# Kernel tuning notes

Hardware: AMD Instinct MI355X
Metric: run time of the kernel (lower is better)

## Reference

```python
import jax, jax.numpy as jnp
import numpy as np

N_NODES = 20000
N_EDGES = 160000
EPS = 1e-5
LEAKY_SLOPE = 0.01


def gcn_conv(x, src, dst, W, b, num_nodes):
    """PyG GCNConv: self-loops + symmetric normalization. out = D^-1/2 A_hat D^-1/2 (x W) + b."""
    h = x @ W  # [N, out]
    loop = jnp.arange(num_nodes, dtype=src.dtype)
    s = jnp.concatenate([src, loop])
    d = jnp.concatenate([dst, loop])
    deg = jax.ops.segment_sum(jnp.ones_like(d, dtype=h.dtype), d, num_segments=num_nodes)
    dinv = jnp.where(deg > 0, jax.lax.rsqrt(jnp.maximum(deg, 1.0)) * jnp.where(deg > 0, 1.0, 0.0), 0.0)
    norm = dinv[s] * dinv[d]  # [E+N]
    msgs = h[s] * norm[:, None]  # gather + scale (memory-bound)
    out = jax.ops.segment_sum(msgs, d, num_segments=num_nodes)
    return out + b


def setup_inputs() -> dict:
    key = jax.random.key(0)
    ks = jax.random.split(key, 8)
    x = jax.random.normal(ks[0], (N_NODES, 1), dtype=jnp.float32)
    edge_index = jax.random.randint(ks[1], (2, N_EDGES), 0, N_NODES, dtype=jnp.int32)
    s = 0.02
    W1 = jax.random.normal(ks[2], (1, 2048), dtype=jnp.float32) * s
    b1 = jnp.zeros((2048,), jnp.float32)
    W2 = jax.random.normal(ks[3], (2048, 1024), dtype=jnp.float32) * s
    b2 = jnp.zeros((1024,), jnp.float32)
    gamma = jnp.ones((1024,), jnp.float32)
    beta = jnp.zeros((1024,), jnp.float32)
    running_mean = jnp.zeros((1024,), jnp.float32)
    running_var = jnp.ones((1024,), jnp.float32)
    lW1 = jax.random.normal(ks[4], (1024, 256), dtype=jnp.float32) * s
    lb1 = jnp.zeros((256,), jnp.float32)
    lW2 = jax.random.normal(ks[5], (256, 124), dtype=jnp.float32) * s
    lb2 = jnp.zeros((124,), jnp.float32)
    return dict(x=x, edge_index=edge_index, W1=W1, b1=b1, W2=W2, b2=b2,
                gamma=gamma, beta=beta, running_mean=running_mean,
                running_var=running_var, lW1=lW1, lb1=lb1, lW2=lW2, lb2=lb2)


def reference(x, edge_index, W1, b1, W2, b2, gamma, beta,
              running_mean, running_var, lW1, lb1, lW2, lb2):
    n = x.shape[0]
    src, dst = edge_index[0], edge_index[1]
    h = gcn_conv(x, src, dst, W1, b1, n)          # GCNConv(1, 2048); dropout is identity in eval
    h = gcn_conv(h, src, dst, W2, b2, n)          # GCNConv(2048, 1024)
    h = (h - running_mean) * (gamma * jax.lax.rsqrt(running_var + EPS)) + beta  # BatchNorm (eval)
    h = h @ lW1 + lb1                              # Linear 1024->256
    h = jnp.where(h >= 0, h, LEAKY_SLOPE * h)      # LeakyReLU
    h = h @ lW2 + lb2                              # Linear 256->124
    return jax.nn.log_softmax(h, axis=1)
```

## Files before the change

### kernel.cpp

```cpp
#include <hip/hip_runtime.h>
#include <math.h>

#define N_NODES 20000
#define N_EDGES 160000
#define EPSB 1e-5f
#define SLOPE 0.01f

typedef __attribute__((ext_vector_type(8))) short short8;
typedef __attribute__((ext_vector_type(4))) float f32x4;

#define OFF_DEG    0
#define OFF_DINV   20000
#define OFF_AGG1   40000
#define OFF_AGG2   60000
#define OFF_CNODE  80000
#define OFF_V      100000
#define OFF_U      101024
#define OFF_R      102048
#define OFF_RU     102304
#define OFF_S      102560
#define OFF_ZEND   102816
#define OFF_BFRAG  102816
#define OFF_RRS    119200

__device__ __forceinline__ unsigned short f2bf(float f) {
    unsigned u = __float_as_uint(f);
    return (unsigned short)((u + 0x7FFFu + ((u >> 16) & 1u)) >> 16);
}

__global__ void K1_deg_v(const int* __restrict__ dst, int* __restrict__ deg,
                         const float* __restrict__ W1, const float* __restrict__ b1,
                         const float* __restrict__ W2,
                         float* __restrict__ v, float* __restrict__ u) {
    int b = blockIdx.x;
    if (b < 256) {
        int k  = (b & 3) * 256 + threadIdx.x;
        int c0 = (b >> 2) * 32;
        float av = 0.f, au = 0.f;
        for (int c = c0; c < c0 + 32; ++c) {
            float w = W2[c * 1024 + k];
            av = fmaf(W1[c], w, av);
            au = fmaf(b1[c], w, au);
        }
        atomicAdd(&v[k], av);
        atomicAdd(&u[k], au);
    } else {
        int e = (b - 256) * 256 + threadIdx.x;
        if (e < N_EDGES) atomicAdd(&deg[dst[e]], 1);
    }
}

__global__ void K2_prep(const int* __restrict__ deg, const float* __restrict__ x,
                        float* __restrict__ dinv, float* __restrict__ agg1,
                        float* __restrict__ cnode) {
    int i = blockIdx.x * blockDim.x + threadIdx.x;
    if (i < N_NODES) {
        float di = rsqrtf((float)(deg[i] + 1));
        dinv[i] = di;
        float d2 = di * di;
        agg1[i]  = d2 * x[i];
        cnode[i] = d2;
    }
}

__global__ void K3_edges1(const int* __restrict__ src, const int* __restrict__ dst,
                          const float* __restrict__ dinv, const float* __restrict__ x,
                          float* __restrict__ agg1, float* __restrict__ cnode) {
    int e = blockIdx.x * blockDim.x + threadIdx.x;
    if (e < N_EDGES) {
        int s = src[e], d = dst[e];
        float nrm = dinv[s] * dinv[d];
        atomicAdd(&agg1[d], nrm * x[s]);
        atomicAdd(&cnode[d], nrm);
    }
}

__global__ void K4_init_rs(const float* __restrict__ dinv, const float* __restrict__ agg1,
                           float* __restrict__ agg2,
                           const float* __restrict__ v, const float* __restrict__ u,
                           const float* __restrict__ gamma, const float* __restrict__ beta,
                           const float* __restrict__ mean, const float* __restrict__ var,
                           const float* __restrict__ b2, const float* __restrict__ lW1,
                           const float* __restrict__ lb1,
                           float* __restrict__ r, float* __restrict__ ru, float* __restrict__ s) {
    int b = blockIdx.x;
    if (b < 79) {
        int i = b * 256 + threadIdx.x;
        if (i < N_NODES) agg2[i] = dinv[i] * dinv[i] * agg1[i];
    } else {
        int m  = threadIdx.x;
        int k0 = (b - 79) * 32;
        float ar = 0.f, aru = 0.f, as = 0.f;
        for (int k = k0; k < k0 + 32; ++k) {
            float g = gamma[k] * rsqrtf(var[k] + EPSB);
            float w = lW1[k * 256 + m];
            ar  = fmaf(v[k] * g, w, ar);
            aru = fmaf(u[k] * g, w, aru);
            as  = fmaf(fmaf(b2[k] - mean[k], g, beta[k]), w, as);
        }
        if (b == 79) as += lb1[m];
        atomicAdd(&r[m], ar);
        atomicAdd(&ru[m], aru);
        atomicAdd(&s[m], as);
    }
}

__global__ void K5_edges2_pad(const int* __restrict__ src, const int* __restrict__ dst,
                              const float* __restrict__ dinv, const float* __restrict__ agg1,
                              float* __restrict__ agg2,
                              const float* __restrict__ lW2,
                              const float* __restrict__ r, const float* __restrict__ ru,
                              const float* __restrict__ s,
                              unsigned short* __restrict__ bfrag, float4* __restrict__ rrs) {
    int b = blockIdx.x;
    if (b < 625) {
        int e = b * 256 + threadIdx.x;
        if (e < N_EDGES) {
            int sn = src[e], d = dst[e];
            atomicAdd(&agg2[d], dinv[sn] * dinv[d] * agg1[sn]);
        }
    } else if (b < 641) {
        int i = (b - 625) * 256 + threadIdx.x;
        int ct = i >> 9, ks = (i >> 6) & 7, lane = i & 63;
        int n = ct * 16 + (lane & 15);
        int kb = ks * 32 + (lane >> 4) * 8;
        union { unsigned short u[8]; short8 v; } pk;
#pragma unroll
        for (int j = 0; j < 8; ++j)
            pk.u[j] = (n < 124) ? f2bf(lW2[(kb + j) * 124 + n]) : (unsigned short)0;
        ((short8*)bfrag)[i] = pk.v;
    } else {
        int i = threadIdx.x;
        rrs[i] = make_float4(r[i], ru[i], s[i], 0.f);
    }
}

#define T_STRIDE 264
__global__ __launch_bounds__(256, 2) void K6_final(
    const float* __restrict__ agg2, const float* __restrict__ cnode,
    const float4* __restrict__ rrs, const short8* __restrict__ bfrag,
    const float* __restrict__ lb2, float* __restrict__ out) {
    __shared__ unsigned short tsh[16 * T_STRIDE];
    __shared__ float a_sh[16], cn_sh[16];
    __shared__ float logits[16 * 132];
    int tid  = threadIdx.x;
    int lane = tid & 63;
    int wave = __builtin_amdgcn_readfirstlane(tid >> 6);
    int row  = lane & 15, quad = lane >> 4;

    short8 bf0[8], bf1[8];
#pragma unroll
    for (int ks = 0; ks < 8; ++ks) {
        bf0[ks] = bfrag[((wave * 2 + 0) * 8 + ks) * 64 + lane];
        bf1[ks] = bfrag[((wave * 2 + 1) * 8 + ks) * 64 + lane];
    }

    for (int it = 0; it < 2; ++it) {
        int node0 = (blockIdx.x * 2 + it) * 16;
        if (tid < 16)      a_sh[tid]       = agg2[node0 + tid];
        else if (tid < 32) cn_sh[tid - 16] = cnode[node0 + tid - 16];
        float4 c = rrs[tid];
        __syncthreads();

#pragma unroll
        for (int n = 0; n < 16; ++n) {
            float t = fmaf(cn_sh[n], c.y, fmaf(a_sh[n], c.x, c.z));
            t = fmaf(SLOPE, fminf(t, 0.f), fmaxf(t, 0.f));
            tsh[n * T_STRIDE + tid] = f2bf(t);
        }
        __syncthreads();

        f32x4 acc0 = {0.f, 0.f, 0.f, 0.f}, acc1 = {0.f, 0.f, 0.f, 0.f};
        const unsigned short* tb = &tsh[row * T_STRIDE + quad * 8];
#pragma unroll
        for (int ks = 0; ks < 8; ++ks) {
            short8 af = *(const short8*)(tb + ks * 32);
            acc0 = __builtin_amdgcn_mfma_f32_16x16x32_bf16(af, bf0[ks], acc0, 0, 0, 0);
            acc1 = __builtin_amdgcn_mfma_f32_16x16x32_bf16(af, bf1[ks], acc1, 0, 0, 0);
        }
        int colbase = wave * 32;
#pragma unroll
        for (int rg = 0; rg < 4; ++rg) {
            int rw = quad * 4 + rg;
            logits[rw * 132 + colbase + row]      = acc0[rg];
            logits[rw * 132 + colbase + 16 + row] = acc1[rg];
        }
        __syncthreads();

        int nd = tid >> 4, sub = tid & 15, c0 = sub * 8;
        int jend = 124 - c0; if (jend > 8) jend = 8;
        float vbuf[8];
        const float* lrow = &logits[nd * 132 + c0];
        float mx = -1e30f;
        for (int j = 0; j < jend; ++j) {
            vbuf[j] = lrow[j] + lb2[c0 + j];
            mx = fmaxf(mx, vbuf[j]);
        }
        mx = fmaxf(mx, __shfl_xor(mx, 1, 16));
        mx = fmaxf(mx, __shfl_xor(mx, 2, 16));
        mx = fmaxf(mx, __shfl_xor(mx, 4, 16));
        mx = fmaxf(mx, __shfl_xor(mx, 8, 16));
        float sm = 0.f;
        for (int j = 0; j < jend; ++j) sm += __expf(vbuf[j] - mx);
        sm += __shfl_xor(sm, 1, 16);
        sm += __shfl_xor(sm, 2, 16);
        sm += __shfl_xor(sm, 4, 16);
        sm += __shfl_xor(sm, 8, 16);
        float lz = mx + __logf(sm);
        float* orow = out + (node0 + nd) * 124 + c0;
        for (int j = 0; j < jend; ++j) orow[j] = vbuf[j] - lz;
    }
}

extern "C" void kernel_launch(void* const* d_in, const int* in_sizes, int n_in,
                              void* d_out, int out_size, void* d_ws, size_t ws_size,
                              hipStream_t stream) {
    const float* x     = (const float*)d_in[0];
    const int*   ei    = (const int*)d_in[1];
    const int*   src   = ei;
    const int*   dst   = ei + N_EDGES;
    const float* W1    = (const float*)d_in[2];
    const float* b1    = (const float*)d_in[3];
    const float* W2    = (const float*)d_in[4];
    const float* b2    = (const float*)d_in[5];
    const float* gamma = (const float*)d_in[6];
    const float* beta  = (const float*)d_in[7];
    const float* rmean = (const float*)d_in[8];
    const float* rvar  = (const float*)d_in[9];
    const float* lW1   = (const float*)d_in[10];
    const float* lb1   = (const float*)d_in[11];
    const float* lW2   = (const float*)d_in[12];
    const float* lb2   = (const float*)d_in[13];
    float* out = (float*)d_out;
    float* ws  = (float*)d_ws;

    int*   deg   = (int*)(ws + OFF_DEG);
    float* dinv  = ws + OFF_DINV;
    float* agg1  = ws + OFF_AGG1;
    float* agg2  = ws + OFF_AGG2;
    float* cnode = ws + OFF_CNODE;
    float* v     = ws + OFF_V;
    float* u     = ws + OFF_U;
    float* r     = ws + OFF_R;
    float* ru    = ws + OFF_RU;
    float* s     = ws + OFF_S;
    unsigned short* bfrag = (unsigned short*)(ws + OFF_BFRAG);
    float4* rrs  = (float4*)(ws + OFF_RRS);

    hipMemsetAsync(ws, 0, OFF_ZEND * sizeof(float), stream);

    K1_deg_v<<<256 + 625, 256, 0, stream>>>(dst, deg, W1, b1, W2, v, u);
    K2_prep<<<79, 256, 0, stream>>>(deg, x, dinv, agg1, cnode);
    K3_edges1<<<625, 256, 0, stream>>>(src, dst, dinv, x, agg1, cnode);
    K4_init_rs<<<79 + 32, 256, 0, stream>>>(dinv, agg1, agg2, v, u, gamma, beta,
                                            rmean, rvar, b2, lW1, lb1, r, ru, s);
    K5_edges2_pad<<<625 + 16 + 1, 256, 0, stream>>>(src, dst, dinv, agg1, agg2,
                                                    lW2, r, ru, s, bfrag, rrs);
    K6_final<<<625, 256, 0, stream>>>(agg2, cnode, rrs, (const short8*)bfrag, lb2, out);
}
```

Baseline: 158.3 us.

## Fuse all stages into one cooperative persistent kernel with grid syncs

Replaces the memset and six separate kernel launches with a single cooperative kernel of 512 blocks that runs every stage in sequence, separated by grid-wide barriers. Zeroing of the accumulators moves into the kernel, and the edge loops and the final tile loop become grid-stride loops over the fixed block count. This is meant to remove per-launch overhead and the gaps between dependent kernels. In exchange it pays for six grid.sync barriers, uses fewer blocks per phase, and requires all 512 blocks to be resident at once (two per CU under the launch bounds).

```diff
diff --git a/kernel.cpp b/kernel.cpp
--- a/kernel.cpp
+++ b/kernel.cpp
@@ -1,10 +1,16 @@
 #include <hip/hip_runtime.h>
+#include <hip/hip_cooperative_groups.h>
 #include <math.h>
+
+namespace cg = cooperative_groups;
 
 #define N_NODES 20000
 #define N_EDGES 160000
 #define EPSB 1e-5f
 #define SLOPE 0.01f
+#define NBLK 512
+#define NTHR 256
+#define GSTRIDE (NBLK * NTHR)
 
 typedef __attribute__((ext_vector_type(8))) short short8;
 typedef __attribute__((ext_vector_type(4))) float f32x4;
@@ -19,23 +25,49 @@
 #define OFF_R      102048
 #define OFF_RU     102304
 #define OFF_S      102560
-#define OFF_ZEND   102816
 #define OFF_BFRAG  102816
 #define OFF_RRS    119200
+
+#define T_STRIDE 264
 
 __device__ __forceinline__ unsigned short f2bf(float f) {
     unsigned u = __float_as_uint(f);
     return (unsigned short)((u + 0x7FFFu + ((u >> 16) & 1u)) >> 16);
 }
 
-__global__ void K1_deg_v(const int* __restrict__ dst, int* __restrict__ deg,
-                         const float* __restrict__ W1, const float* __restrict__ b1,
-                         const float* __restrict__ W2,
-                         float* __restrict__ v, float* __restrict__ u) {
-    int b = blockIdx.x;
-    if (b < 256) {
-        int k  = (b & 3) * 256 + threadIdx.x;
-        int c0 = (b >> 2) * 32;
+__global__ __launch_bounds__(256, 2) void KAll(
+    const float* __restrict__ x, const int* __restrict__ src, const int* __restrict__ dst,
+    const float* __restrict__ W1, const float* __restrict__ b1, const float* __restrict__ W2,
+    const float* __restrict__ b2, const float* __restrict__ gamma, const float* __restrict__ beta,
+    const float* __restrict__ mean, const float* __restrict__ var,
+    const float* __restrict__ lW1, const float* __restrict__ lb1,
+    const float* __restrict__ lW2, const float* __restrict__ lb2,
+    int* __restrict__ deg, float* __restrict__ dinv, float* __restrict__ agg1,
+    float* __restrict__ agg2, float* __restrict__ cnode,
+    float* __restrict__ v, float* __restrict__ u,
+    float* __restrict__ r, float* __restrict__ ru, float* __restrict__ s,
+    unsigned short* __restrict__ bfrag, float4* __restrict__ rrs,
+    float* __restrict__ out)
+{
+    cg::grid_group grid = cg::this_grid();
+    __shared__ unsigned short tsh[16 * T_STRIDE];
+    __shared__ float a_sh[16], cn_sh[16];
+    __shared__ float logits[16 * 132];
+
+    const int b   = blockIdx.x;
+    const int tid = threadIdx.x;
+    const int gix = b * NTHR + tid;
+
+    if (gix < N_NODES) deg[gix] = 0;
+    if (gix < 1024) { v[gix] = 0.f; u[gix] = 0.f; }
+    else if (gix < 1280) { int m = gix - 1024; r[m] = 0.f; ru[m] = 0.f; s[m] = 0.f; }
+    grid.sync();
+
+    for (int e = gix; e < N_EDGES; e += GSTRIDE) atomicAdd(&deg[dst[e]], 1);
+    if (b >= 256) {
+        int bb = b - 256;
+        int k  = (bb & 3) * 256 + tid;
+        int c0 = (bb >> 2) * 32;
         float av = 0.f, au = 0.f;
         for (int c = c0; c < c0 + 32; ++c) {
             float w = W2[c * 1024 + k];
@@ -44,52 +76,29 @@
         }
         atomicAdd(&v[k], av);
         atomicAdd(&u[k], au);
-    } else {
-        int e = (b - 256) * 256 + threadIdx.x;
-        if (e < N_EDGES) atomicAdd(&deg[dst[e]], 1);
-    }
-}
-
-__global__ void K2_prep(const int* __restrict__ deg, const float* __restrict__ x,
-                        float* __restrict__ dinv, float* __restrict__ agg1,
-                        float* __restrict__ cnode) {
-    int i = blockIdx.x * blockDim.x + threadIdx.x;
-    if (i < N_NODES) {
-        float di = rsqrtf((float)(deg[i] + 1));
-        dinv[i] = di;
+    }
+    grid.sync();
+
+    if (gix < N_NODES) {
+        float di = rsqrtf((float)(deg[gix] + 1));
+        dinv[gix] = di;
         float d2 = di * di;
-        agg1[i]  = d2 * x[i];
-        cnode[i] = d2;
-    }
-}
-
-__global__ void K3_edges1(const int* __restrict__ src, const int* __restrict__ dst,
-                          const float* __restrict__ dinv, const float* __restrict__ x,
-                          float* __restrict__ agg1, float* __restrict__ cnode) {
-    int e = blockIdx.x * blockDim.x + threadIdx.x;
-    if (e < N_EDGES) {
-        int s = src[e], d = dst[e];
-        float nrm = dinv[s] * dinv[d];
-        atomicAdd(&agg1[d], nrm * x[s]);
+        agg1[gix]  = d2 * x[gix];
+        cnode[gix] = d2;
+    }
+    grid.sync();
+
+    for (int e = gix; e < N_EDGES; e += GSTRIDE) {
+        int sn = src[e], d = dst[e];
+        float nrm = dinv[sn] * dinv[d];
+        atomicAdd(&agg1[d], nrm * x[sn]);
         atomicAdd(&cnode[d], nrm);
     }
-}
-
-__global__ void K4_init_rs(const float* __restrict__ dinv, const float* __restrict__ agg1,
-                           float* __restrict__ agg2,
-                           const float* __restrict__ v, const float* __restrict__ u,
-                           const float* __restrict__ gamma, const float* __restrict__ beta,
-                           const float* __restrict__ mean, const float* __restrict__ var,
-                           const float* __restrict__ b2, const float* __restrict__ lW1,
-                           const float* __restrict__ lb1,
-                           float* __restrict__ r, float* __restrict__ ru, float* __restrict__ s) {
-    int b = blockIdx.x;
-    if (b < 79) {
-        int i = b * 256 + threadIdx.x;
-        if (i < N_NODES) agg2[i] = dinv[i] * dinv[i] * agg1[i];
-    } else {
-        int m  = threadIdx.x;
-        int k0 = (b - 79) * 32;
+    grid.sync();
+
+    if (gix < N_NODES) agg2[gix] = dinv[gix] * dinv[gix] * agg1[gix];
+    if (b >= 480) {
+        int bb = b - 480, m = tid, k0 = bb * 32;
         float ar = 0.f, aru = 0.f, as = 0.f;
         for (int k = k0; k < k0 + 32; ++k) {
             float g = gamma[k] * rsqrtf(var[k] + EPSB);
@@ -98,52 +107,32 @@
             aru = fmaf(u[k] * g, w, aru);
             as  = fmaf(fmaf(b2[k] - mean[k], g, beta[k]), w, as);
         }
-        if (b == 79) as += lb1[m];
+        if (bb == 0) as += lb1[m];
         atomicAdd(&r[m], ar);
         atomicAdd(&ru[m], aru);
         atomicAdd(&s[m], as);
     }
-}
-
-__global__ void K5_edges2_pad(const int* __restrict__ src, const int* __restrict__ dst,
-                              const float* __restrict__ dinv, const float* __restrict__ agg1,
-                              float* __restrict__ agg2,
-                              const float* __restrict__ lW2,
-                              const float* __restrict__ r, const float* __restrict__ ru,
-                              const float* __restrict__ s,
-                              unsigned short* __restrict__ bfrag, float4* __restrict__ rrs) {
-    int b = blockIdx.x;
-    if (b < 625) {
-        int e = b * 256 + threadIdx.x;
-        if (e < N_EDGES) {
-            int sn = src[e], d = dst[e];
-            atomicAdd(&agg2[d], dinv[sn] * dinv[d] * agg1[sn]);
-        }
-    } else if (b < 641) {
-        int i = (b - 625) * 256 + threadIdx.x;
+    grid.sync();
+
+    for (int e = gix; e < N_EDGES; e += GSTRIDE) {
+        int sn = src[e], d = dst[e];
+        atomicAdd(&agg2[d], dinv[sn] * dinv[d] * agg1[sn]);
+    }
+    if (b >= 480 && b < 496) {
+        int i = (b - 480) * 256 + tid;
         int ct = i >> 9, ks = (i >> 6) & 7, lane = i & 63;
-        int n = ct * 16 + (lane & 15);
+        int n  = ct * 16 + (lane & 15);
         int kb = ks * 32 + (lane >> 4) * 8;
-        union { unsigned short u[8]; short8 v; } pk;
+        union { unsigned short u8[8]; short8 v8; } pk;
 #pragma unroll
         for (int j = 0; j < 8; ++j)
-            pk.u[j] = (n < 124) ? f2bf(lW2[(kb + j) * 124 + n]) : (unsigned short)0;
-        ((short8*)bfrag)[i] = pk.v;
-    } else {
-        int i = threadIdx.x;
-        rrs[i] = make_float4(r[i], ru[i], s[i], 0.f);
-    }
-}
-
-#define T_STRIDE 264
-__global__ __launch_bounds__(256, 2) void K6_final(
-    const float* __restrict__ agg2, const float* __restrict__ cnode,
-    const float4* __restrict__ rrs, const short8* __restrict__ bfrag,
-    const float* __restrict__ lb2, float* __restrict__ out) {
-    __shared__ unsigned short tsh[16 * T_STRIDE];
-    __shared__ float a_sh[16], cn_sh[16];
-    __shared__ float logits[16 * 132];
-    int tid  = threadIdx.x;
+            pk.u8[j] = (n < 124) ? f2bf(lW2[(kb + j) * 124 + n]) : (unsigned short)0;
+        ((short8*)bfrag)[i] = pk.v8;
+    } else if (b == 496) {
+        rrs[tid] = make_float4(r[tid], ru[tid], s[tid], 0.f);
+    }
+    grid.sync();
+
     int lane = tid & 63;
     int wave = __builtin_amdgcn_readfirstlane(tid >> 6);
     int row  = lane & 15, quad = lane >> 4;
@@ -151,15 +140,17 @@
     short8 bf0[8], bf1[8];
 #pragma unroll
     for (int ks = 0; ks < 8; ++ks) {
-        bf0[ks] = bfrag[((wave * 2 + 0) * 8 + ks) * 64 + lane];
-        bf1[ks] = bfrag[((wave * 2 + 1) * 8 + ks) * 64 + lane];
-    }
-
-    for (int it = 0; it < 2; ++it) {
-        int node0 = (blockIdx.x * 2 + it) * 16;
+        bf0[ks] = ((const short8*)bfrag)[((wave * 2 + 0) * 8 + ks) * 64 + lane];
+        bf1[ks] = ((const short8*)bfrag)[((wave * 2 + 1) * 8 + ks) * 64 + lane];
+    }
+    float4 c = rrs[tid];
+
+    for (int it = 0; it < 3; ++it) {
+        int tile = it * NBLK + b;
+        if (tile >= 1250) break;
+        int node0 = tile * 16;
         if (tid < 16)      a_sh[tid]       = agg2[node0 + tid];
         else if (tid < 32) cn_sh[tid - 16] = cnode[node0 + tid - 16];
-        float4 c = rrs[tid];
         __syncthreads();
 
 #pragma unroll
@@ -247,14 +238,13 @@
     unsigned short* bfrag = (unsigned short*)(ws + OFF_BFRAG);
     float4* rrs  = (float4*)(ws + OFF_RRS);
 
-    hipMemsetAsync(ws, 0, OFF_ZEND * sizeof(float), stream);
-
-    K1_deg_v<<<256 + 625, 256, 0, stream>>>(dst, deg, W1, b1, W2, v, u);
-    K2_prep<<<79, 256, 0, stream>>>(deg, x, dinv, agg1, cnode);
-    K3_edges1<<<625, 256, 0, stream>>>(src, dst, dinv, x, agg1, cnode);
-    K4_init_rs<<<79 + 32, 256, 0, stream>>>(dinv, agg1, agg2, v, u, gamma, beta,
-                                            rmean, rvar, b2, lW1, lb1, r, ru, s);
-    K5_edges2_pad<<<625 + 16 + 1, 256, 0, stream>>>(src, dst, dinv, agg1, agg2,
-                                                    lW2, r, ru, s, bfrag, rrs);
-    K6_final<<<625, 256, 0, stream>>>(agg2, cnode, rrs, (const short8*)bfrag, lb2, out);
+    void* args[] = {
+        (void*)&x, (void*)&src, (void*)&dst, (void*)&W1, (void*)&b1, (void*)&W2,
+        (void*)&b2, (void*)&gamma, (void*)&beta, (void*)&rmean, (void*)&rvar,
+        (void*)&lW1, (void*)&lb1, (void*)&lW2, (void*)&lb2,
+        (void*)&deg, (void*)&dinv, (void*)&agg1, (void*)&agg2, (void*)&cnode,
+        (void*)&v, (void*)&u, (void*)&r, (void*)&ru, (void*)&s,
+        (void*)&bfrag, (void*)&rrs, (void*)&out
+    };
+    hipLaunchCooperativeKernel((const void*)KAll, dim3(NBLK), dim3(NTHR), args, 0, stream);
 }
```

Result: slower. 497.1 us (+214.1%).

## Merge prep and self-loop init kernels to cut launches, shrink memset region

Applied to the files above, without the earlier changes.

Reduces the chain from six kernels to five. The node prep is merged with the r/ru/s projection, and the edge pass is merged with the bfrag packing. The layer-2 self-loop term is no longer written into agg2 beforehand; the final kernel adds it on the fly from dinv and agg1. Workspace is reordered so only the atomically accumulated buffers (deg, agg2, v, u, r, ru, s) are zeroed, shrinking the memset. The price is a few extra loads in the final kernel.

```diff
diff --git a/kernel.cpp b/kernel.cpp
--- a/kernel.cpp
+++ b/kernel.cpp
@@ -10,18 +10,20 @@
 typedef __attribute__((ext_vector_type(4))) float f32x4;
 
 #define OFF_DEG    0
-#define OFF_DINV   20000
-#define OFF_AGG1   40000
-#define OFF_AGG2   60000
-#define OFF_CNODE  80000
-#define OFF_V      100000
-#define OFF_U      101024
-#define OFF_R      102048
-#define OFF_RU     102304
-#define OFF_S      102560
-#define OFF_ZEND   102816
+#define OFF_AGG2   20000
+#define OFF_V      40000
+#define OFF_U      41024
+#define OFF_R      42048
+#define OFF_RU     42304
+#define OFF_S      42560
+#define OFF_ZEND   42816
+#define OFF_DINV   42816
+#define OFF_AGG1   62816
+#define OFF_CNODE  82816
 #define OFF_BFRAG  102816
 #define OFF_RRS    119200
+
+#define T_STRIDE 264
 
 __device__ __forceinline__ unsigned short f2bf(float f) {
     unsigned u = __float_as_uint(f);
@@ -33,9 +35,13 @@
                          const float* __restrict__ W2,
                          float* __restrict__ v, float* __restrict__ u) {
     int b = blockIdx.x;
-    if (b < 256) {
-        int k  = (b & 3) * 256 + threadIdx.x;
-        int c0 = (b >> 2) * 32;
+    if (b < 625) {
+        int e = b * 256 + threadIdx.x;
+        atomicAdd(&deg[dst[e]], 1);
+    } else {
+        int bb = b - 625;
+        int k  = (bb & 3) * 256 + threadIdx.x;
+        int c0 = (bb >> 2) * 32;
         float av = 0.f, au = 0.f;
         for (int c = c0; c < c0 + 32; ++c) {
             float w = W2[c * 1024 + k];
@@ -44,39 +50,12 @@
         }
         atomicAdd(&v[k], av);
         atomicAdd(&u[k], au);
-    } else {
-        int e = (b - 256) * 256 + threadIdx.x;
-        if (e < N_EDGES) atomicAdd(&deg[dst[e]], 1);
-    }
-}
-
-__global__ void K2_prep(const int* __restrict__ deg, const float* __restrict__ x,
-                        float* __restrict__ dinv, float* __restrict__ agg1,
-                        float* __restrict__ cnode) {
-    int i = blockIdx.x * blockDim.x + threadIdx.x;
-    if (i < N_NODES) {
-        float di = rsqrtf((float)(deg[i] + 1));
-        dinv[i] = di;
-        float d2 = di * di;
-        agg1[i]  = d2 * x[i];
-        cnode[i] = d2;
-    }
-}
-
-__global__ void K3_edges1(const int* __restrict__ src, const int* __restrict__ dst,
-                          const float* __restrict__ dinv, const float* __restrict__ x,
-                          float* __restrict__ agg1, float* __restrict__ cnode) {
-    int e = blockIdx.x * blockDim.x + threadIdx.x;
-    if (e < N_EDGES) {
-        int s = src[e], d = dst[e];
-        float nrm = dinv[s] * dinv[d];
-        atomicAdd(&agg1[d], nrm * x[s]);
-        atomicAdd(&cnode[d], nrm);
-    }
-}
-
-__global__ void K4_init_rs(const float* __restrict__ dinv, const float* __restrict__ agg1,
-                           float* __restrict__ agg2,
+    }
+}
+
+__global__ void K2_prep_rs(const int* __restrict__ deg, const float* __restrict__ x,
+                           float* __restrict__ dinv, float* __restrict__ agg1,
+                           float* __restrict__ cnode,
                            const float* __restrict__ v, const float* __restrict__ u,
                            const float* __restrict__ gamma, const float* __restrict__ beta,
                            const float* __restrict__ mean, const float* __restrict__ var,
@@ -86,10 +65,15 @@
     int b = blockIdx.x;
     if (b < 79) {
         int i = b * 256 + threadIdx.x;
-        if (i < N_NODES) agg2[i] = dinv[i] * dinv[i] * agg1[i];
-    } else {
-        int m  = threadIdx.x;
-        int k0 = (b - 79) * 32;
+        if (i < N_NODES) {
+            float di = rsqrtf((float)(deg[i] + 1));
+            dinv[i] = di;
+            float d2 = di * di;
+            agg1[i]  = d2 * x[i];
+            cnode[i] = d2;
+        }
+    } else {
+        int bb = b - 79, m = threadIdx.x, k0 = bb * 32;
         float ar = 0.f, aru = 0.f, as = 0.f;
         for (int k = k0; k < k0 + 32; ++k) {
             float g = gamma[k] * rsqrtf(var[k] + EPSB);
@@ -98,46 +82,57 @@
             aru = fmaf(u[k] * g, w, aru);
             as  = fmaf(fmaf(b2[k] - mean[k], g, beta[k]), w, as);
         }
-        if (b == 79) as += lb1[m];
+        if (bb == 0) as += lb1[m];
         atomicAdd(&r[m], ar);
         atomicAdd(&ru[m], aru);
         atomicAdd(&s[m], as);
     }
 }
 
-__global__ void K5_edges2_pad(const int* __restrict__ src, const int* __restrict__ dst,
+__global__ void K3_edges1_bfrag(const int* __restrict__ src, const int* __restrict__ dst,
+                                const float* __restrict__ dinv, const float* __restrict__ x,
+                                float* __restrict__ agg1, float* __restrict__ cnode,
+                                const float* __restrict__ lW2,
+                                unsigned short* __restrict__ bfrag) {
+    int b = blockIdx.x;
+    if (b < 625) {
+        int e = b * 256 + threadIdx.x;
+        int sn = src[e], d = dst[e];
+        float nrm = dinv[sn] * dinv[d];
+        atomicAdd(&agg1[d], nrm * x[sn]);
+        atomicAdd(&cnode[d], nrm);
+    } else {
+        int i = (b - 625) * 256 + threadIdx.x;
+        int ct = i >> 9, ks = (i >> 6) & 7, lane = i & 63;
+        int n  = ct * 16 + (lane & 15);
+        int kb = ks * 32 + (lane >> 4) * 8;
+        union { unsigned short u8[8]; short8 v8; } pk;
+#pragma unroll
+        for (int j = 0; j < 8; ++j)
+            pk.u8[j] = (n < 124) ? f2bf(lW2[(kb + j) * 124 + n]) : (unsigned short)0;
+        ((short8*)bfrag)[i] = pk.v8;
+    }
+}
+
+__global__ void K4_edges2_rrs(const int* __restrict__ src, const int* __restrict__ dst,
                               const float* __restrict__ dinv, const float* __restrict__ agg1,
                               float* __restrict__ agg2,
-                              const float* __restrict__ lW2,
                               const float* __restrict__ r, const float* __restrict__ ru,
-                              const float* __restrict__ s,
-                              unsigned short* __restrict__ bfrag, float4* __restrict__ rrs) {
+                              const float* __restrict__ s, float4* __restrict__ rrs) {
     int b = blockIdx.x;
     if (b < 625) {
         int e = b * 256 + threadIdx.x;
-        if (e < N_EDGES) {
-            int sn = src[e], d = dst[e];
-            atomicAdd(&agg2[d], dinv[sn] * dinv[d] * agg1[sn]);
-        }
-    } else if (b < 641) {
-        int i = (b - 625) * 256 + threadIdx.x;
-        int ct = i >> 9, ks = (i >> 6) & 7, lane = i & 63;
-        int n = ct * 16 + (lane & 15);
-        int kb = ks * 32 + (lane >> 4) * 8;
-        union { unsigned short u[8]; short8 v; } pk;
-#pragma unroll
-        for (int j = 0; j < 8; ++j)
-            pk.u[j] = (n < 124) ? f2bf(lW2[(kb + j) * 124 + n]) : (unsigned short)0;
-        ((short8*)bfrag)[i] = pk.v;
+        int sn = src[e], d = dst[e];
+        atomicAdd(&agg2[d], dinv[sn] * dinv[d] * agg1[sn]);
     } else {
         int i = threadIdx.x;
         rrs[i] = make_float4(r[i], ru[i], s[i], 0.f);
     }
 }
 
-#define T_STRIDE 264
-__global__ __launch_bounds__(256, 2) void K6_final(
-    const float* __restrict__ agg2, const float* __restrict__ cnode,
+__global__ __launch_bounds__(256, 2) void KF_final(
+    const float* __restrict__ agg2, const float* __restrict__ dinv,
+    const float* __restrict__ agg1, const float* __restrict__ cnode,
     const float4* __restrict__ rrs, const short8* __restrict__ bfrag,
     const float* __restrict__ lb2, float* __restrict__ out) {
     __shared__ unsigned short tsh[16 * T_STRIDE];
@@ -154,12 +149,17 @@
         bf0[ks] = bfrag[((wave * 2 + 0) * 8 + ks) * 64 + lane];
         bf1[ks] = bfrag[((wave * 2 + 1) * 8 + ks) * 64 + lane];
     }
+    float4 c = rrs[tid];
 
     for (int it = 0; it < 2; ++it) {
         int node0 = (blockIdx.x * 2 + it) * 16;
-        if (tid < 16)      a_sh[tid]       = agg2[node0 + tid];
-        else if (tid < 32) cn_sh[tid - 16] = cnode[node0 + tid - 16];
-        float4 c = rrs[tid];
+        if (tid < 16) {
+            int n = node0 + tid;
+            float di = dinv[n];
+            a_sh[tid] = fmaf(di * di, agg1[n], agg2[n]);
+        } else if (tid < 32) {
+            cn_sh[tid - 16] = cnode[node0 + tid - 16];
+        }
         __syncthreads();
 
 #pragma unroll
@@ -235,26 +235,25 @@
     float* ws  = (float*)d_ws;
 
     int*   deg   = (int*)(ws + OFF_DEG);
-    float* dinv  = ws + OFF_DINV;
-    float* agg1  = ws + OFF_AGG1;
     float* agg2  = ws + OFF_AGG2;
-    float* cnode = ws + OFF_CNODE;
     float* v     = ws + OFF_V;
     float* u     = ws + OFF_U;
     float* r     = ws + OFF_R;
     float* ru    = ws + OFF_RU;
     float* s     = ws + OFF_S;
+    float* dinv  = ws + OFF_DINV;
+    float* agg1  = ws + OFF_AGG1;
+    float* cnode = ws + OFF_CNODE;
     unsigned short* bfrag = (unsigned short*)(ws + OFF_BFRAG);
     float4* rrs  = (float4*)(ws + OFF_RRS);
 
     hipMemsetAsync(ws, 0, OFF_ZEND * sizeof(float), stream);
 
-    K1_deg_v<<<256 + 625, 256, 0, stream>>>(dst, deg, W1, b1, W2, v, u);
-    K2_prep<<<79, 256, 0, stream>>>(deg, x, dinv, agg1, cnode);
-    K3_edges1<<<625, 256, 0, stream>>>(src, dst, dinv, x, agg1, cnode);
-    K4_init_rs<<<79 + 32, 256, 0, stream>>>(dinv, agg1, agg2, v, u, gamma, beta,
+    K1_deg_v<<<625 + 256, 256, 0, stream>>>(dst, deg, W1, b1, W2, v, u);
+    K2_prep_rs<<<79 + 32, 256, 0, stream>>>(deg, x, dinv, agg1, cnode, v, u, gamma, beta,
                                             rmean, rvar, b2, lW1, lb1, r, ru, s);
-    K5_edges2_pad<<<625 + 16 + 1, 256, 0, stream>>>(src, dst, dinv, agg1, agg2,
-                                                    lW2, r, ru, s, bfrag, rrs);
-    K6_final<<<625, 256, 0, stream>>>(agg2, cnode, rrs, (const short8*)bfrag, lb2, out);
-}
+    K3_edges1_bfrag<<<625 + 16, 256, 0, stream>>>(src, dst, dinv, x, agg1, cnode, lW2, bfrag);
+    K4_edges2_rrs<<<625 + 1, 256, 0, stream>>>(src, dst, dinv, agg1, agg2, r, ru, s, rrs);
+    KF_final<<<625, 256, 0, stream>>>(agg2, dinv, agg1, cnode, rrs,
+                                      (const short8*)bfrag, lb2, out);
+}
```

Measured after the change: 161.3 us. About the same (+1.9%).
